# Kernel optimization log

Hardware: AMD Instinct MI355X
Metric: run time of the kernel (lower is better)

Reference implementation:

```python
import jax, jax.numpy as jnp
import numpy as np

N_NODES = 10000
N_EDGES = 320000
K_STEPS = 2          # max_diffusion_step
N_SUPPORTS = 2
C_IN = 64
C_OUT = 64
BATCH = 64
NUM_MATRICES = K_STEPS * N_SUPPORTS + 1  # 5


def setup_inputs() -> dict:
    key = jax.random.key(0)
    k_x, k_v, k_t, k_b, k_r, k_c = jax.random.split(key, 6)
    x = jax.random.normal(k_x, (BATCH, N_NODES, C_IN), dtype=jnp.float32)
    # edge values scaled ~1/avg_degree so row sums are O(1), like a random-walk matrix
    edge_vals = jax.random.uniform(k_v, (N_SUPPORTS, N_EDGES), dtype=jnp.float32) / 32.0
    Theta = jax.random.normal(k_t, (NUM_MATRICES * C_IN, C_OUT), dtype=jnp.float32) * 0.05
    bias = jax.random.normal(k_b, (C_OUT,), dtype=jnp.float32) * 0.01
    edge_rows = jax.random.randint(k_r, (N_SUPPORTS, N_EDGES), 0, N_NODES, dtype=jnp.int32)
    edge_cols = jax.random.randint(k_c, (N_SUPPORTS, N_EDGES), 0, N_NODES, dtype=jnp.int32)
    return {"x": x, "edge_vals": edge_vals, "Theta": Theta, "bias": bias,
            "edge_rows": edge_rows, "edge_cols": edge_cols}


def _spmm(rows, cols, vals, m, n):
    # sparse [n,n] @ dense [n, d] via gather + segment_sum
    return jax.ops.segment_sum(vals[:, None] * m[cols], rows, num_segments=n)


def reference(x, edge_vals, Theta, bias, edge_rows, edge_cols):
    b, n, c = x.shape
    # Faithful to source: raw reshape (n, c*b) of a (b,n,c) tensor (row-major)
    x0 = x.reshape(n, c * b)
    xs = [x0]
    for s in range(N_SUPPORTS):
        rows, cols, vals = edge_rows[s], edge_cols[s], edge_vals[s]
        x_km1, x_km2 = x0, x0
        x1 = _spmm(rows, cols, vals, x0, n)
        xs.append(x1)
        x_km1, x_km2 = x1, x0
        for _ in range(2, K_STEPS + 1):
            x2 = 2.0 * _spmm(rows, cols, vals, x_km1, n) - x_km2
            xs.append(x2)
            x_km1, x_km2 = x2, x_km1
    xcat = jnp.stack(xs, axis=0)                      # (M, n, c*b)
    xcat = xcat.reshape(len(xs), n, c, b)             # (M, n, c, b)
    xcat = xcat.transpose(3, 1, 2, 0)                 # (b, n, c, M)
    xcat = xcat.reshape(b, n, c * len(xs))            # (b, n, c*M)
    out = jnp.matmul(xcat, Theta) + bias              # (b, n, c_out)
    return out
```

## Files before the change

kernel.cpp:

```cpp
#include <hip/hip_runtime.h>
#include <stdint.h>
#include <stddef.h>

#define NN 10000
#define NE 320000
#define NSUP 2
#define CB 4096
#define RPS 10016
#define NCHUNK 32
#define CHUNK_B 256
#define PEPAD 400016
#define NXCD 8

typedef unsigned int uint32;
typedef unsigned short u16;
typedef __attribute__((ext_vector_type(8))) short bf16x8;
typedef __attribute__((ext_vector_type(8))) u16 u16x8;
typedef __attribute__((ext_vector_type(4))) float f32x4;

__device__ __forceinline__ float bf2f(u16 u) {
    union { unsigned int i; float f; } v; v.i = ((unsigned int)u) << 16; return v.f;
}
__device__ __forceinline__ u16 f2bf(float f) {
    union { float f; unsigned int i; } v; v.f = f;
    unsigned int u = v.i;
    return (u16)((u + 0x7fffu + ((u >> 16) & 1u)) >> 16);
}

__global__ __launch_bounds__(256) void k_transpose(const float* __restrict__ x,
                                                   u16* __restrict__ xT) {
    __shared__ float tile[4160];
    const int row = blockIdx.x;
    const int tid = threadIdx.x;
    const f32x4* src = (const f32x4*)(x + (size_t)row * CB);
    #pragma unroll
    for (int q = 0; q < 4; ++q) {
        f32x4 v = src[tid + q * 256];
        int j0 = (tid + q * 256) * 4;
        #pragma unroll
        for (int r = 0; r < 4; ++r) {
            int j = j0 + r;
            tile[j + (j >> 6)] = v[r];
        }
    }
    __syncthreads();
    u16x8 o0, o1;
    #pragma unroll
    for (int jj = 0; jj < 16; ++jj) {
        int j = tid * 16 + jj;
        int b = j >> 6, c = j & 63;
        u16 t = f2bf(tile[c * 65 + b]);
        if (jj < 8) o0[jj] = t; else o1[jj - 8] = t;
    }
    u16x8* dst = (u16x8*)(xT + (size_t)row * CB + tid * 16);
    dst[0] = o0; dst[1] = o1;
}

__global__ __launch_bounds__(256) void k_zero(int* __restrict__ p, int n) {
    int i = blockIdx.x * 256 + threadIdx.x;
    if (i < n) p[i] = 0;
}

__global__ __launch_bounds__(256) void k_hist(const int* __restrict__ rows,
                                              int* __restrict__ counts) {
    int g = blockIdx.x * 256 + threadIdx.x;
    if (g >= NSUP * NE) return;
    int s = g / NE;
    atomicAdd(&counts[s * RPS + rows[g]], 1);
}

__global__ __launch_bounds__(1024) void k_scan(const int* __restrict__ counts,
                                               int* __restrict__ rowptr,
                                               int* __restrict__ cursor) {
    const int s = blockIdx.x;
    const int tid = threadIdx.x;
    __shared__ int buf[1024];
    __shared__ int carry_s;
    if (tid == 0) carry_s = 0;
    __syncthreads();
    for (int base = 0; base < NN; base += 1024) {
        int i = base + tid;
        int v = (i < NN) ? ((counts[s * RPS + i] + 7) & ~7) : 0;
        buf[tid] = v;
        __syncthreads();
        for (int off = 1; off < 1024; off <<= 1) {
            int t = (tid >= off) ? buf[tid - off] : 0;
            __syncthreads();
            buf[tid] += t;
            __syncthreads();
        }
        int carry = carry_s;
        int excl = carry + buf[tid] - v;
        if (i < NN) { rowptr[s * RPS + i] = excl; cursor[s * RPS + i] = excl; }
        __syncthreads();
        if (tid == 1023) carry_s = carry + buf[1023];
        __syncthreads();
    }
    if (tid == 0) rowptr[s * RPS + NN] = carry_s;
}

__global__ __launch_bounds__(256) void k_scatter(const int* __restrict__ rows,
                                                 const int* __restrict__ cols,
                                                 const float* __restrict__ vals,
                                                 int* __restrict__ cursor,
                                                 uint2* __restrict__ pedges) {
    int g = blockIdx.x * 256 + threadIdx.x;
    if (g >= NSUP * NE) return;
    int s = g / NE;
    int r = rows[g];
    int pos = atomicAdd(&cursor[s * RPS + r], 1);
    uint2 p;
    p.x = (unsigned int)cols[g];
    p.y = __float_as_uint(vals[g]);
    pedges[(size_t)s * PEPAD + pos] = p;
}

__global__ __launch_bounds__(256) void k_theta(const float* __restrict__ Theta,
                                               u16* __restrict__ thetaFrag) {
    int idx = blockIdx.x * 256 + threadIdx.x;
    if (idx >= 20480) return;
    int j = idx & 7;
    int lane = (idx >> 3) & 63;
    int ct = (idx >> 9) & 3;
    int ks = idx >> 11;
    int kp = ks * 32 + ((lane >> 4) << 3) + j;
    int m = kp >> 6, c = kp & 63;
    int co = ct * 16 + (lane & 15);
    thetaFrag[idx] = f2bf(Theta[(c * 5 + m) * 64 + co]);
}

#define GATHER8(M)                                                              \
    _Pragma("unroll")                                                           \
    for (int j = 0; j < 8; ++j)                                                 \
        u[j] = *(const uint32*)(srcb + (((M)[j].x << 13) + cb));

#define PREFETCH8(M, blk)                                                       \
    {                                                                           \
        const uint2* pn_ = pe + (size_t)(blk) * 8;                              \
        _Pragma("unroll")                                                       \
        for (int j = 0; j < 8; ++j) (M)[j] = pn_[j];                            \
    }

#define FMA8(M)                                                                 \
    _Pragma("unroll")                                                           \
    for (int j = 0; j < 8; ++j) {                                               \
        float v_ = __uint_as_float((M)[j].y);                                   \
        a0 = fmaf(v_, __uint_as_float(u[j] << 16), a0);                         \
        a1 = fmaf(v_, __uint_as_float(u[j] & 0xffff0000u), a1);                 \
    }

__device__ __forceinline__ void spmm_core(const char* __restrict__ srcb,
                                          const uint2* __restrict__ pe,
                                          int nblk, uint32 cb,
                                          float& a0, float& a1) {
    uint2 ma[8], mb[8];
    uint32 u[8];
    PREFETCH8(ma, 0)
    int b = 0;
    for (; b + 2 <= nblk; b += 2) {
        GATHER8(ma)
        PREFETCH8(mb, b + 1)
        FMA8(ma)
        GATHER8(mb)
        PREFETCH8(ma, b + 2)
        FMA8(mb)
    }
    if (b < nblk) {
        GATHER8(ma)
        FMA8(ma)
    }
}

__global__ __launch_bounds__(256) void k_spmm1(const u16* __restrict__ src,
                                               u16* __restrict__ dst0,
                                               u16* __restrict__ dst1,
                                               const int* __restrict__ rowptr,
                                               const uint2* __restrict__ pedges) {
    const int bx = blockIdx.x;
    const int xcd = bx & (NXCD - 1);
    const int l = bx >> 3;
    const int cwx = l / (2 * (NN / 4));
    const int r2 = l - cwx * (2 * (NN / 4));
    const int chunk = xcd * (NCHUNK / NXCD) + cwx;
    const int s = r2 & 1;
    const int quad = r2 >> 1;
    const int wave = threadIdx.x >> 6, lane = threadIdx.x & 63;
    const int row = quad * 4 + wave;
    const uint32 cb = (uint32)chunk * CHUNK_B + (uint32)lane * 4;
    const int* rp = rowptr + s * RPS;
    const int e0 = __builtin_amdgcn_readfirstlane(rp[row]);
    const int e1 = __builtin_amdgcn_readfirstlane(rp[row + 1]);
    const uint2* pe = pedges + (size_t)s * PEPAD + e0;
    float a0 = 0.f, a1 = 0.f;
    spmm_core((const char*)src, pe, (e1 - e0) >> 3, cb, a0, a1);
    u16* dst = s ? dst1 : dst0;
    uint32 o = (uint32)f2bf(a0) | ((uint32)f2bf(a1) << 16);
    __builtin_nontemporal_store(o, (uint32*)((char*)dst + (size_t)row * (CB * 2) + cb));
}

__global__ __launch_bounds__(256) void k_spmm2(const u16* __restrict__ src,
                                               const u16* __restrict__ aux,
                                               u16* __restrict__ dst,
                                               const int* __restrict__ rowptr,
                                               const uint2* __restrict__ pedges) {
    const int bx = blockIdx.x;
    const int xcd = bx & (NXCD - 1);
    const int l = bx >> 3;
    const int cwx = l / (NN / 4);
    const int quad = l - cwx * (NN / 4);
    const int chunk = xcd * (NCHUNK / NXCD) + cwx;
    const int wave = threadIdx.x >> 6, lane = threadIdx.x & 63;
    const int row = quad * 4 + wave;
    const uint32 cb = (uint32)chunk * CHUNK_B + (uint32)lane * 4;
    const int e0 = __builtin_amdgcn_readfirstlane(rowptr[row]);
    const int e1 = __builtin_amdgcn_readfirstlane(rowptr[row + 1]);
    const uint2* pe = pedges + e0;
    float a0 = 0.f, a1 = 0.f;
    spmm_core((const char*)src, pe, (e1 - e0) >> 3, cb, a0, a1);
    const size_t rowoff = (size_t)row * (CB * 2) + cb;
    uint32 av = __builtin_nontemporal_load((const uint32*)((const char*)aux + rowoff));
    float c0 = 2.f * a0 - __uint_as_float(av << 16);
    float c1 = 2.f * a1 - __uint_as_float(av & 0xffff0000u);
    uint32 o = (uint32)f2bf(c0) | ((uint32)f2bf(c1) << 16);
    __builtin_nontemporal_store(o, (uint32*)((char*)dst + rowoff));
}

__global__ __launch_bounds__(256) void k_gemm(const u16* __restrict__ mats,
                                              const u16* __restrict__ thetaFrag,
                                              const float* __restrict__ bias,
                                              float* __restrict__ out) {
    __shared__ u16 th[20480];
    const int tid = threadIdx.x;
    #pragma unroll
    for (int q = 0; q < 10; ++q) {
        int idx = tid * 8 + q * 2048;
        *(u16x8*)&th[idx] = *(const u16x8*)&thetaFrag[idx];
    }
    __syncthreads();
    const int wave = tid >> 6, lane = tid & 63;
    const int node = blockIdx.x * 4 + wave;
    const int l15 = lane & 15, lhi = lane >> 4;

    f32x4 acc[4][4];
    #pragma unroll
    for (int ct = 0; ct < 4; ++ct) {
        float bv = bias[ct * 16 + l15];
        #pragma unroll
        for (int bt = 0; bt < 4; ++bt) {
            acc[bt][ct][0] = bv; acc[bt][ct][1] = bv; acc[bt][ct][2] = bv; acc[bt][ct][3] = bv;
        }
    }
    #pragma unroll
    for (int ks = 0; ks < 10; ++ks) {
        const int m = ks >> 1;
        const int c0 = ((ks & 1) << 5) + (lhi << 3);
        const u16* mbase = mats + (size_t)m * ((size_t)NN * CB) + (size_t)node * CB;
        bf16x8 af[4];
        #pragma unroll
        for (int bt = 0; bt < 4; ++bt)
            af[bt] = *(const bf16x8*)(mbase + (bt * 16 + l15) * 64 + c0);
        #pragma unroll
        for (int ct = 0; ct < 4; ++ct) {
            bf16x8 bf = *(const bf16x8*)&th[((ks * 4 + ct) * 64 + lane) * 8];
            #pragma unroll
            for (int bt = 0; bt < 4; ++bt)
                acc[bt][ct] = __builtin_amdgcn_mfma_f32_16x16x32_bf16(af[bt], bf, acc[bt][ct], 0, 0, 0);
        }
    }
    #pragma unroll
    for (int bt = 0; bt < 4; ++bt)
        #pragma unroll
        for (int ct = 0; ct < 4; ++ct)
            #pragma unroll
            for (int r = 0; r < 4; ++r) {
                int b = bt * 16 + lhi * 4 + r;
                int co = ct * 16 + l15;
                out[(size_t)b * (NN * 64) + (size_t)node * 64 + co] = acc[bt][ct][r];
            }
}

extern "C" void kernel_launch(void* const* d_in, const int* in_sizes, int n_in,
                              void* d_out, int out_size, void* d_ws, size_t ws_size,
                              hipStream_t stream) {
    const float* x         = (const float*)d_in[0];
    const float* edge_vals = (const float*)d_in[1];
    const float* Theta     = (const float*)d_in[2];
    const float* bias      = (const float*)d_in[3];
    const int*   edge_rows = (const int*)d_in[4];
    const int*   edge_cols = (const int*)d_in[5];
    float* out = (float*)d_out;

    uint8_t* ws = (uint8_t*)d_ws;
    const size_t MAT_E = (size_t)NN * CB;
    const size_t MAT_B = MAT_E * 2;

    u16* mats      = (u16*)ws;
    u16* thetaFrag = (u16*)(ws + 5 * MAT_B);
    uint8_t* p = ws + 5 * MAT_B + 40960;
    int* counts = (int*)p;  p += (size_t)NSUP * RPS * 4;
    int* rowptr = (int*)p;  p += (size_t)NSUP * RPS * 4;
    int* cursor = (int*)p;  p += (size_t)NSUP * RPS * 4;
    p = (uint8_t*)(((uintptr_t)p + 255) & ~(uintptr_t)255);
    uint2* pedges = (uint2*)p;

    u16* m0 = mats;
    u16* m1 = mats + MAT_E;
    u16* m2 = mats + 2 * MAT_E;
    u16* m3 = mats + 3 * MAT_E;
    u16* m4 = mats + 4 * MAT_E;

    k_transpose<<<NN, 256, 0, stream>>>(x, m0);
    k_zero<<<(NSUP * RPS + 255) / 256, 256, 0, stream>>>(counts, NSUP * RPS);
    k_zero<<<(NSUP * PEPAD * 2 + 255) / 256, 256, 0, stream>>>((int*)pedges, NSUP * PEPAD * 2);
    k_hist<<<(NSUP * NE) / 256, 256, 0, stream>>>(edge_rows, counts);
    k_scan<<<NSUP, 1024, 0, stream>>>(counts, rowptr, cursor);
    k_scatter<<<(NSUP * NE) / 256, 256, 0, stream>>>(edge_rows, edge_cols, edge_vals,
                                                     cursor, pedges);
    k_theta<<<80, 256, 0, stream>>>(Theta, thetaFrag);

    k_spmm1<<<NCHUNK * (NN / 4) * 2, 256, 0, stream>>>(m0, m1, m3, rowptr, pedges);
    k_spmm2<<<NCHUNK * (NN / 4), 256, 0, stream>>>(m1, m0, m2, rowptr, pedges);
    k_spmm2<<<NCHUNK * (NN / 4), 256, 0, stream>>>(m3, m0, m4, rowptr + RPS, pedges + PEPAD);

    k_gemm<<<NN / 4, 256, 0, stream>>>(mats, thetaFrag, bias, out);
}
```

Before: 911.1 us.

## Deepen SpMM gather pipeline to three stages and merge second-step launches

The SpMM inner loop now keeps three 8-edge blocks in flight instead of two, so more gathers are outstanding while FMAs run. The two second-order diffusion launches (one per support) are merged into a single launch that picks source, destination and edge list by block index, removing a kernel boundary and letting both supports fill the GPU together. The deeper pipeline raises register use and may lower occupancy, and the remainder-handling logic is more complex.

```diff
diff --git a/kernel.cpp b/kernel.cpp
--- a/kernel.cpp
+++ b/kernel.cpp
@@ -129,45 +129,54 @@
     thetaFrag[idx] = f2bf(Theta[(c * 5 + m) * 64 + co]);
 }
 
-#define GATHER8(M)                                                              \
-    _Pragma("unroll")                                                           \
-    for (int j = 0; j < 8; ++j)                                                 \
-        u[j] = *(const uint32*)(srcb + (((M)[j].x << 13) + cb));
-
-#define PREFETCH8(M, blk)                                                       \
+#define PRE8(E, blk)                                                            \
     {                                                                           \
         const uint2* pn_ = pe + (size_t)(blk) * 8;                              \
         _Pragma("unroll")                                                       \
-        for (int j = 0; j < 8; ++j) (M)[j] = pn_[j];                            \
-    }
-
-#define FMA8(M)                                                                 \
+        for (int j = 0; j < 8; ++j) (E)[j] = pn_[j];                            \
+    }
+
+#define GAT8(G, E)                                                              \
+    _Pragma("unroll")                                                           \
+    for (int j = 0; j < 8; ++j)                                                 \
+        (G)[j] = *(const uint32*)(srcb + (((E)[j].x << 13) + cb));
+
+#define FMA8(G, E)                                                              \
     _Pragma("unroll")                                                           \
     for (int j = 0; j < 8; ++j) {                                               \
-        float v_ = __uint_as_float((M)[j].y);                                   \
-        a0 = fmaf(v_, __uint_as_float(u[j] << 16), a0);                         \
-        a1 = fmaf(v_, __uint_as_float(u[j] & 0xffff0000u), a1);                 \
+        float v_ = __uint_as_float((E)[j].y);                                   \
+        a0 = fmaf(v_, __uint_as_float((G)[j] << 16), a0);                       \
+        a1 = fmaf(v_, __uint_as_float((G)[j] & 0xffff0000u), a1);               \
     }
 
 __device__ __forceinline__ void spmm_core(const char* __restrict__ srcb,
                                           const uint2* __restrict__ pe,
                                           int nblk, uint32 cb,
                                           float& a0, float& a1) {
-    uint2 ma[8], mb[8];
-    uint32 u[8];
-    PREFETCH8(ma, 0)
-    int b = 0;
-    for (; b + 2 <= nblk; b += 2) {
-        GATHER8(ma)
-        PREFETCH8(mb, b + 1)
-        FMA8(ma)
-        GATHER8(mb)
-        PREFETCH8(ma, b + 2)
-        FMA8(mb)
-    }
-    if (b < nblk) {
-        GATHER8(ma)
-        FMA8(ma)
+    uint2 e0[8], e1[8], e2[8];
+    uint32 g0[8], g1[8], g2[8];
+    if (nblk >= 3) {
+        PRE8(e0, 0) GAT8(g0, e0)
+        PRE8(e1, 1) GAT8(g1, e1)
+        PRE8(e2, 2) GAT8(g2, e2)
+        int b = 0;
+        for (; b + 6 <= nblk; b += 3) {
+            FMA8(g0, e0) PRE8(e0, b + 3) GAT8(g0, e0)
+            FMA8(g1, e1) PRE8(e1, b + 4) GAT8(g1, e1)
+            FMA8(g2, e2) PRE8(e2, b + 5) GAT8(g2, e2)
+        }
+        const int r = nblk - b;
+        FMA8(g0, e0)
+        if (r >= 4) { PRE8(e0, b + 3) GAT8(g0, e0) }
+        FMA8(g1, e1)
+        if (r == 5) { PRE8(e1, b + 4) GAT8(g1, e1) }
+        FMA8(g2, e2)
+        if (r >= 4) FMA8(g0, e0)
+        if (r == 5) FMA8(g1, e1)
+    } else {
+        for (int t = 0; t < nblk; ++t) {
+            PRE8(e0, t) GAT8(g0, e0) FMA8(g0, e0)
+        }
     }
 }
 
@@ -198,30 +207,37 @@
     __builtin_nontemporal_store(o, (uint32*)((char*)dst + (size_t)row * (CB * 2) + cb));
 }
 
-__global__ __launch_bounds__(256) void k_spmm2(const u16* __restrict__ src,
+__global__ __launch_bounds__(256) void k_spmm2(const u16* __restrict__ src0,
+                                               const u16* __restrict__ src1,
                                                const u16* __restrict__ aux,
-                                               u16* __restrict__ dst,
+                                               u16* __restrict__ dst0,
+                                               u16* __restrict__ dst1,
                                                const int* __restrict__ rowptr,
                                                const uint2* __restrict__ pedges) {
     const int bx = blockIdx.x;
     const int xcd = bx & (NXCD - 1);
     const int l = bx >> 3;
-    const int cwx = l / (NN / 4);
-    const int quad = l - cwx * (NN / 4);
+    const int cwx = l / (2 * (NN / 4));
+    const int r2 = l - cwx * (2 * (NN / 4));
     const int chunk = xcd * (NCHUNK / NXCD) + cwx;
+    const int s = r2 / (NN / 4);
+    const int quad = r2 - s * (NN / 4);
     const int wave = threadIdx.x >> 6, lane = threadIdx.x & 63;
     const int row = quad * 4 + wave;
     const uint32 cb = (uint32)chunk * CHUNK_B + (uint32)lane * 4;
-    const int e0 = __builtin_amdgcn_readfirstlane(rowptr[row]);
-    const int e1 = __builtin_amdgcn_readfirstlane(rowptr[row + 1]);
-    const uint2* pe = pedges + e0;
+    const int* rp = rowptr + s * RPS;
+    const int e0 = __builtin_amdgcn_readfirstlane(rp[row]);
+    const int e1 = __builtin_amdgcn_readfirstlane(rp[row + 1]);
+    const uint2* pe = pedges + (size_t)s * PEPAD + e0;
+    const char* srcb = (const char*)(s ? src1 : src0);
     float a0 = 0.f, a1 = 0.f;
-    spmm_core((const char*)src, pe, (e1 - e0) >> 3, cb, a0, a1);
+    spmm_core(srcb, pe, (e1 - e0) >> 3, cb, a0, a1);
     const size_t rowoff = (size_t)row * (CB * 2) + cb;
     uint32 av = __builtin_nontemporal_load((const uint32*)((const char*)aux + rowoff));
     float c0 = 2.f * a0 - __uint_as_float(av << 16);
     float c1 = 2.f * a1 - __uint_as_float(av & 0xffff0000u);
     uint32 o = (uint32)f2bf(c0) | ((uint32)f2bf(c1) << 16);
+    u16* dst = s ? dst1 : dst0;
     __builtin_nontemporal_store(o, (uint32*)((char*)dst + rowoff));
 }
 
@@ -319,8 +335,8 @@
     k_theta<<<80, 256, 0, stream>>>(Theta, thetaFrag);
 
     k_spmm1<<<NCHUNK * (NN / 4) * 2, 256, 0, stream>>>(m0, m1, m3, rowptr, pedges);
-    k_spmm2<<<NCHUNK * (NN / 4), 256, 0, stream>>>(m1, m0, m2, rowptr, pedges);
-    k_spmm2<<<NCHUNK * (NN / 4), 256, 0, stream>>>(m3, m0, m4, rowptr + RPS, pedges + PEPAD);
+    k_spmm2<<<NCHUNK * (NN / 4) * 2, 256, 0, stream>>>(m1, m3, m0, m2, m4,
+                                                       rowptr, pedges);
 
     k_gemm<<<NN / 4, 256, 0, stream>>>(mats, thetaFrag, bias, out);
 }
```

New measurement: 962.7 us. 5.7% more time.
